# Optimization experiments

Measured on AMD Instinct MI355X. Metric: run time of the kernel, lower is better.

Reference implementation:

```python
import jax, jax.numpy as jnp
import numpy as np

N = 100000      # nodes
E = 1280000     # edges
D_IN = 64       # in_channels
D_OUT = 64      # out_channels
D_EDGE = 16     # edge_dim
NEG_SLOPE = 0.01  # torch F.leaky_relu default


def setup_inputs() -> dict:
    key = jax.random.key(0)
    ks = jax.random.split(key, 8)
    x = jax.random.normal(ks[0], (N, D_IN), dtype=jnp.float32)
    edge_attr = jax.random.normal(ks[1], (E, D_EDGE), dtype=jnp.float32)
    src = jax.random.randint(ks[2], (E,), 0, N, dtype=jnp.int32)
    dst = jax.random.randint(ks[3], (E,), 0, N, dtype=jnp.int32)
    # parameters (xavier-like scale)
    W1 = jax.random.normal(ks[4], (D_OUT, D_IN + D_EDGE), dtype=jnp.float32) * (2.0 / (D_OUT + D_IN + D_EDGE)) ** 0.5
    W2 = jax.random.normal(ks[5], (D_OUT, D_IN), dtype=jnp.float32) * (2.0 / (D_OUT + D_IN)) ** 0.5
    attn = jax.random.normal(ks[6], (D_OUT + D_IN,), dtype=jnp.float32) * (2.0 / (1 + D_OUT + D_IN)) ** 0.5
    bias = jnp.zeros((D_OUT,), dtype=jnp.float32)
    return {"x": x, "edge_attr": edge_attr, "src": src, "dst": dst,
            "W1": W1, "W2": W2, "attn": attn, "bias": bias}


def reference(x, edge_attr, src, dst, W1, W2, attn, bias):
    # node transform: lin2
    x_t = x @ W2.T                                    # [N, D_OUT]
    # per-edge gathers
    x_l = x[src]                                      # [E, D_IN]
    x_r = x[dst]                                      # [E, D_IN]
    # lin1 on [x_l || edge_attr]
    f_srt = jnp.concatenate([x_l, edge_attr], axis=-1) @ W1.T   # [E, D_OUT]
    e = jax.nn.leaky_relu(jnp.concatenate([f_srt, x_r], axis=-1), NEG_SLOPE)  # [E, D_OUT+D_IN]
    logits = e @ attn                                 # [E]
    # edge_softmax over destination-node segments
    seg_max = jax.ops.segment_max(logits, dst, num_segments=N)
    seg_max = jnp.where(jnp.isfinite(seg_max), seg_max, 0.0)
    expd = jnp.exp(logits - seg_max[dst])             # [E]
    denom = jax.ops.segment_sum(expd, dst, num_segments=N)
    alpha = expd / denom[dst]                         # [E]  (dropout p=0 -> identity)
    # scatter-sum aggregation: sum_e alpha_e * x_t[src_e] into dst
    msgs = x_t[src] * alpha[:, None]                  # [E, D_OUT]
    h = jax.ops.segment_sum(msgs, dst, num_segments=N)
    return h + bias
```

## Files before the change

kernel.cpp:

```cpp
#include <hip/hip_runtime.h>

#define D 64
#define D_EDGE 16
#define NEG 0.01f

typedef unsigned int  uint32;
typedef unsigned short ushort16;

__device__ __forceinline__ float leaky(float v) { return fmaxf(v, NEG * v); }

__device__ __forceinline__ ushort16 f2bf(float f) {
    uint32 b = __float_as_uint(f);
    uint32 r = b + 0x7fffu + ((b >> 16) & 1u);
    return (ushort16)(r >> 16);
}
__device__ __forceinline__ float bf2f(ushort16 u) {
    return __uint_as_float(((uint32)u) << 16);
}
__device__ __forceinline__ float bf_lo(uint32 w) { return __uint_as_float(w << 16); }
__device__ __forceinline__ float bf_hi(uint32 w) { return __uint_as_float(w & 0xffff0000u); }

__global__ __launch_bounds__(256) void node_kernel(
    const float* __restrict__ x, const float* __restrict__ W1,
    const float* __restrict__ W2,
    ushort16* __restrict__ Abf, ushort16* __restrict__ xtb, int N_)
{
    __shared__ float xs[64][68];
    uint32* sA = (uint32*)&xs[0][0];
    uint32* sX = sA + 64 * 33;

    const int tid = threadIdx.x;
    const int b0  = blockIdx.x * 64;

    for (int idx = tid; idx < 64 * 16; idx += 256) {
        const int rr = idx >> 4, cc = idx & 15;
        float4 v = make_float4(0.f, 0.f, 0.f, 0.f);
        if (b0 + rr < N_) v = ((const float4*)(x + (size_t)(b0 + rr) * D))[cc];
        *(float4*)&xs[rr][cc * 4] = v;
    }
    __syncthreads();

    const int lane = tid & 63;
    const int q    = __builtin_amdgcn_readfirstlane(tid >> 6);

    float4 xr[16];
#pragma unroll
    for (int i = 0; i < 16; i++) xr[i] = *(const float4*)&xs[lane][4 * i];
    __syncthreads();

    float a_prev = 0.f, b_prev = 0.f;
#pragma unroll
    for (int kk = 0; kk < 16; kk++) {
        const int k = q * 16 + kk;
        const float4* w2r = (const float4*)(W2 + (size_t)k * 64);
        const float4* w1r = (const float4*)(W1 + (size_t)k * 80);
        float a = 0.f, b = 0.f;
#pragma unroll
        for (int j = 0; j < 16; j++) {
            float4 w = w2r[j];
            a += xr[j].x * w.x + xr[j].y * w.y + xr[j].z * w.z + xr[j].w * w.w;
            float4 u = w1r[j];
            b += xr[j].x * u.x + xr[j].y * u.y + xr[j].z * u.z + xr[j].w * u.w;
        }
        if (kk & 1) {
            const int pr = k >> 1;
            sX[lane * 33 + pr] = (uint32)f2bf(a_prev) | ((uint32)f2bf(a) << 16);
            sA[lane * 33 + pr] = (uint32)f2bf(b_prev) | ((uint32)f2bf(b) << 16);
        } else {
            a_prev = a; b_prev = b;
        }
    }
    __syncthreads();

    uint32* Au = (uint32*)Abf;
    uint32* Xu = (uint32*)xtb;
    const size_t gbase = (size_t)b0 * 32;
    for (int base = tid * 4; base < 2048; base += 1024) {
        const int nn = base >> 5, cc = base & 31;
        if (b0 + nn < N_) {
            const uint32* ra = sA + nn * 33 + cc;
            const uint32* rx = sX + nn * 33 + cc;
            uint4 va = make_uint4(ra[0], ra[1], ra[2], ra[3]);
            uint4 vx = make_uint4(rx[0], rx[1], rx[2], rx[3]);
            *(uint4*)(Au + gbase + base) = va;
            *(uint4*)(Xu + gbase + base) = vx;
        }
    }
}

__global__ __launch_bounds__(256) void hist_kernel(
    const int* __restrict__ dst, int* __restrict__ cnt, int E_)
{
    int i = blockIdx.x * 256 + threadIdx.x;
    if (i < E_) atomicAdd(cnt + dst[i], 1);
}

__global__ __launch_bounds__(256) void scan1(
    const int* __restrict__ cnt, int* __restrict__ part, int N_)
{
    __shared__ int sm[256];
    const int b = blockIdx.x, t = threadIdx.x;
    const int i0 = b * 1024 + t * 4;
    int s = 0;
    if (i0     < N_) s += cnt[i0];
    if (i0 + 1 < N_) s += cnt[i0 + 1];
    if (i0 + 2 < N_) s += cnt[i0 + 2];
    if (i0 + 3 < N_) s += cnt[i0 + 3];
    sm[t] = s; __syncthreads();
    for (int off = 128; off > 0; off >>= 1) {
        if (t < off) sm[t] += sm[t + off];
        __syncthreads();
    }
    if (t == 0) part[b] = sm[0];
}

__global__ __launch_bounds__(256) void scan2(int* __restrict__ part, int nb)
{
    __shared__ int sm[256];
    const int t = threadIdx.x;
    int v = (t < nb) ? part[t] : 0;
    sm[t] = v; __syncthreads();
    for (int off = 1; off < 256; off <<= 1) {
        int a = (t >= off) ? sm[t - off] : 0;
        __syncthreads();
        sm[t] += a;
        __syncthreads();
    }
    if (t < nb) part[t] = sm[t] - v;
}

__global__ __launch_bounds__(256) void scan3(
    const int* __restrict__ cnt, const int* __restrict__ part,
    int* __restrict__ rowst, int N_)
{
    __shared__ int sm[256];
    const int b = blockIdx.x, t = threadIdx.x;
    const int i0 = b * 1024 + t * 4;
    int c0 = 0, c1 = 0, c2 = 0, c3 = 0;
    if (i0     < N_) c0 = cnt[i0];
    if (i0 + 1 < N_) c1 = cnt[i0 + 1];
    if (i0 + 2 < N_) c2 = cnt[i0 + 2];
    if (i0 + 3 < N_) c3 = cnt[i0 + 3];
    const int s = c0 + c1 + c2 + c3;
    sm[t] = s; __syncthreads();
    for (int off = 1; off < 256; off <<= 1) {
        int a = (t >= off) ? sm[t - off] : 0;
        __syncthreads();
        sm[t] += a;
        __syncthreads();
    }
    const int base = part[b] + (sm[t] - s);
    if (i0     < N_) rowst[i0]     = base;
    if (i0 + 1 < N_) rowst[i0 + 1] = base + c0;
    if (i0 + 2 < N_) rowst[i0 + 2] = base + c0 + c1;
    if (i0 + 3 < N_) rowst[i0 + 3] = base + c0 + c1 + c2;
}

__global__ __launch_bounds__(256) void edge_kernel(
    const float* __restrict__ edge_attr, const int* __restrict__ src,
    const int* __restrict__ dst, const float* __restrict__ W1,
    const float* __restrict__ attn, const ushort16* __restrict__ Abf,
    int* __restrict__ rowpos, int2* __restrict__ SP, int E_)
{
    const int e = blockIdx.x * 256 + threadIdx.x;
    if (e >= E_) return;

    const int s = src[e];
    const int d = dst[e];

    uint32 Ad[32];
    {
        const uint4* Ap = (const uint4*)(Abf + (size_t)s * D);
#pragma unroll
        for (int i = 0; i < 8; i++) *(uint4*)(Ad + 4 * i) = Ap[i];
    }
    float Ef[16];
    {
        const float4* Ep = (const float4*)(edge_attr + (size_t)e * D_EDGE);
#pragma unroll
        for (int i = 0; i < 4; i++) *(float4*)(Ef + 4 * i) = Ep[i];
    }

    float v = 0.f;
#pragma unroll
    for (int j = 0; j < 32; ++j) {
        const float4* w0 = (const float4*)(W1 + (2 * j) * 80 + 64);
        const float4* w1 = (const float4*)(W1 + (2 * j + 1) * 80 + 64);
        float4 p0 = w0[0], p1 = w0[1], p2 = w0[2], p3 = w0[3];
        float4 q0 = w1[0], q1 = w1[1], q2 = w1[2], q3 = w1[3];

        float g0 = bf_lo(Ad[j]);
        float g1 = bf_hi(Ad[j]);

        g0 = fmaf(Ef[ 0], p0.x, g0); g1 = fmaf(Ef[ 0], q0.x, g1);
        g0 = fmaf(Ef[ 1], p0.y, g0); g1 = fmaf(Ef[ 1], q0.y, g1);
        g0 = fmaf(Ef[ 2], p0.z, g0); g1 = fmaf(Ef[ 2], q0.z, g1);
        g0 = fmaf(Ef[ 3], p0.w, g0); g1 = fmaf(Ef[ 3], q0.w, g1);
        g0 = fmaf(Ef[ 4], p1.x, g0); g1 = fmaf(Ef[ 4], q1.x, g1);
        g0 = fmaf(Ef[ 5], p1.y, g0); g1 = fmaf(Ef[ 5], q1.y, g1);
        g0 = fmaf(Ef[ 6], p1.z, g0); g1 = fmaf(Ef[ 6], q1.z, g1);
        g0 = fmaf(Ef[ 7], p1.w, g0); g1 = fmaf(Ef[ 7], q1.w, g1);
        g0 = fmaf(Ef[ 8], p2.x, g0); g1 = fmaf(Ef[ 8], q2.x, g1);
        g0 = fmaf(Ef[ 9], p2.y, g0); g1 = fmaf(Ef[ 9], q2.y, g1);
        g0 = fmaf(Ef[10], p2.z, g0); g1 = fmaf(Ef[10], q2.z, g1);
        g0 = fmaf(Ef[11], p2.w, g0); g1 = fmaf(Ef[11], q2.w, g1);
        g0 = fmaf(Ef[12], p3.x, g0); g1 = fmaf(Ef[12], q3.x, g1);
        g0 = fmaf(Ef[13], p3.y, g0); g1 = fmaf(Ef[13], q3.y, g1);
        g0 = fmaf(Ef[14], p3.z, g0); g1 = fmaf(Ef[14], q3.z, g1);
        g0 = fmaf(Ef[15], p3.w, g0); g1 = fmaf(Ef[15], q3.w, g1);

        v = fmaf(leaky(g0), attn[2 * j],     v);
        v = fmaf(leaky(g1), attn[2 * j + 1], v);
    }

    const float p = __expf(v);
    const int pos = atomicAdd(rowpos + d, 1);
    SP[pos] = make_int2(s, __float_as_int(p));
}

__global__ __launch_bounds__(256) void agg_kernel(
    const ushort16* __restrict__ xtb, const int2* __restrict__ SP,
    const int* __restrict__ rowend, const float* __restrict__ bias,
    float* __restrict__ out, int N_)
{
    const int n    = blockIdx.x * 4 + (threadIdx.x >> 6);
    const int lane = threadIdx.x & 63;
    if (n >= N_) return;
    const int half = lane >> 5;
    const int c    = lane & 31;

    const int end   = rowend[n];
    const int start = n ? rowend[n - 1] : 0;
    const uint32* X = (const uint32*)xtb;

    float accx = 0.f, accy = 0.f, den = 0.f;
    int i = start;
    for (; i + 7 < end; i += 8) {
        int2 A0 = SP[i+0], A1 = SP[i+1], A2 = SP[i+2], A3 = SP[i+3];
        int2 A4 = SP[i+4], A5 = SP[i+5], A6 = SP[i+6], A7 = SP[i+7];
        int   r0 = half ? A1.x : A0.x;  float p0 = __int_as_float(half ? A1.y : A0.y);
        int   r1 = half ? A3.x : A2.x;  float p1 = __int_as_float(half ? A3.y : A2.y);
        int   r2 = half ? A5.x : A4.x;  float p2 = __int_as_float(half ? A5.y : A4.y);
        int   r3 = half ? A7.x : A6.x;  float p3 = __int_as_float(half ? A7.y : A6.y);
        uint32 u0 = X[(size_t)r0 * 32 + c];
        uint32 u1 = X[(size_t)r1 * 32 + c];
        uint32 u2 = X[(size_t)r2 * 32 + c];
        uint32 u3 = X[(size_t)r3 * 32 + c];
        accx = fmaf(p0, bf_lo(u0), accx); accy = fmaf(p0, bf_hi(u0), accy);
        accx = fmaf(p1, bf_lo(u1), accx); accy = fmaf(p1, bf_hi(u1), accy);
        accx = fmaf(p2, bf_lo(u2), accx); accy = fmaf(p2, bf_hi(u2), accy);
        accx = fmaf(p3, bf_lo(u3), accx); accy = fmaf(p3, bf_hi(u3), accy);
        den += (p0 + p1) + (p2 + p3);
    }
    for (; i < end; i++) {
        int2 a = SP[i];
        if (half == 0) {
            float p = __int_as_float(a.y);
            uint32 u = X[(size_t)a.x * 32 + c];
            accx = fmaf(p, bf_lo(u), accx);
            accy = fmaf(p, bf_hi(u), accy);
            den += p;
        }
    }
    accx += __shfl_xor(accx, 32, 64);
    accy += __shfl_xor(accy, 32, 64);
    den  += __shfl_xor(den,  32, 64);

    if (half == 0) {
        const float sc = den > 0.f ? 1.f / den : 0.f;
        const float2 bb = *(const float2*)(bias + 2 * c);
        float2 o;
        o.x = fmaf(accx, sc, bb.x);
        o.y = fmaf(accy, sc, bb.y);
        *(float2*)(out + (size_t)n * D + 2 * c) = o;
    }
}

extern "C" void kernel_launch(void* const* d_in, const int* in_sizes, int n_in,
                              void* d_out, int out_size, void* d_ws, size_t ws_size,
                              hipStream_t stream)
{
    const float* x         = (const float*)d_in[0];
    const float* edge_attr = (const float*)d_in[1];
    const int*   src       = (const int*)d_in[2];
    const int*   dst       = (const int*)d_in[3];
    const float* W1        = (const float*)d_in[4];
    const float* W2        = (const float*)d_in[5];
    const float* attn      = (const float*)d_in[6];
    const float* bias      = (const float*)d_in[7];
    float* out = (float*)d_out;

    const int N_ = in_sizes[0] / D;
    const int E_ = in_sizes[2];

    char* w = (char*)d_ws;
    ushort16* Abf  = (ushort16*)w;  w += (size_t)N_ * D * sizeof(ushort16);
    ushort16* xtb  = (ushort16*)w;  w += (size_t)N_ * D * sizeof(ushort16);
    int2*     SP   = (int2*)w;      w += (size_t)E_ * sizeof(int2);
    int*      rowst= (int*)w;       w += (size_t)N_ * sizeof(int);
    int*      cnt  = (int*)w;       w += (size_t)N_ * sizeof(int);
    int*      part = (int*)w;

    hipMemsetAsync(cnt, 0, (size_t)N_ * sizeof(int), stream);

    const int NB1 = (N_ + 1023) / 1024;

    hist_kernel<<<(E_ + 255) / 256, 256, 0, stream>>>(dst, cnt, E_);
    scan1<<<NB1, 256, 0, stream>>>(cnt, part, N_);
    scan2<<<1, 256, 0, stream>>>(part, NB1);
    scan3<<<NB1, 256, 0, stream>>>(cnt, part, rowst, N_);

    node_kernel<<<(N_ + 63) / 64, 256, 0, stream>>>(x, W1, W2, Abf, xtb, N_);

    edge_kernel<<<(E_ + 255) / 256, 256, 0, stream>>>(edge_attr, src, dst, W1,
                                                      attn, Abf, rowst, SP, E_);

    agg_kernel<<<(N_ + 3) / 4, 256, 0, stream>>>(xtb, SP, rowst, bias, out, N_);
}
```

Measured before the change: 414.2 us.

## Fold block-prefix scan into scan3 and split edge FMA chains

Removes the separate single-block scan2 launch by having every scan3 block redundantly scan the partial sums in shared memory, which saves one kernel launch and its dependency gap. The edge kernel's per-channel dot products are split into two independent FMA chains with two attention accumulators, to shorten the dependent-FMA latency. It also adds a min-blocks launch bound of 4 to cap register use. The trade-offs are slightly different floating-point summation order and possible register spills under the tighter bound.

Result: no change. 412.2 us (-0.5%).

```diff
diff --git a/kernel.cpp b/kernel.cpp
--- a/kernel.cpp
+++ b/kernel.cpp
@@ -114,27 +114,24 @@
     if (t == 0) part[b] = sm[0];
 }
 
-__global__ __launch_bounds__(256) void scan2(int* __restrict__ part, int nb)
-{
-    __shared__ int sm[256];
-    const int t = threadIdx.x;
-    int v = (t < nb) ? part[t] : 0;
-    sm[t] = v; __syncthreads();
-    for (int off = 1; off < 256; off <<= 1) {
-        int a = (t >= off) ? sm[t - off] : 0;
-        __syncthreads();
-        sm[t] += a;
-        __syncthreads();
-    }
-    if (t < nb) part[t] = sm[t] - v;
-}
-
 __global__ __launch_bounds__(256) void scan3(
     const int* __restrict__ cnt, const int* __restrict__ part,
-    int* __restrict__ rowst, int N_)
-{
+    int* __restrict__ rowst, int N_, int nb)
+{
+    __shared__ int sp[256];
     __shared__ int sm[256];
     const int b = blockIdx.x, t = threadIdx.x;
+
+    sp[t] = (t < nb) ? part[t] : 0;
+    __syncthreads();
+    for (int off = 1; off < 256; off <<= 1) {
+        int a = (t >= off) ? sp[t - off] : 0;
+        __syncthreads();
+        sp[t] += a;
+        __syncthreads();
+    }
+    const int pbase = (b > 0) ? sp[b - 1] : 0;
+
     const int i0 = b * 1024 + t * 4;
     int c0 = 0, c1 = 0, c2 = 0, c3 = 0;
     if (i0     < N_) c0 = cnt[i0];
@@ -149,14 +146,14 @@
         sm[t] += a;
         __syncthreads();
     }
-    const int base = part[b] + (sm[t] - s);
+    const int base = pbase + (sm[t] - s);
     if (i0     < N_) rowst[i0]     = base;
     if (i0 + 1 < N_) rowst[i0 + 1] = base + c0;
     if (i0 + 2 < N_) rowst[i0 + 2] = base + c0 + c1;
     if (i0 + 3 < N_) rowst[i0 + 3] = base + c0 + c1 + c2;
 }
 
-__global__ __launch_bounds__(256) void edge_kernel(
+__global__ __launch_bounds__(256, 4) void edge_kernel(
     const float* __restrict__ edge_attr, const int* __restrict__ src,
     const int* __restrict__ dst, const float* __restrict__ W1,
     const float* __restrict__ attn, const ushort16* __restrict__ Abf,
@@ -181,7 +178,7 @@
         for (int i = 0; i < 4; i++) *(float4*)(Ef + 4 * i) = Ep[i];
     }
 
-    float v = 0.f;
+    float va = 0.f, vb = 0.f;
 #pragma unroll
     for (int j = 0; j < 32; ++j) {
         const float4* w0 = (const float4*)(W1 + (2 * j) * 80 + 64);
@@ -189,31 +186,35 @@
         float4 p0 = w0[0], p1 = w0[1], p2 = w0[2], p3 = w0[3];
         float4 q0 = w1[0], q1 = w1[1], q2 = w1[2], q3 = w1[3];
 
-        float g0 = bf_lo(Ad[j]);
-        float g1 = bf_hi(Ad[j]);
-
-        g0 = fmaf(Ef[ 0], p0.x, g0); g1 = fmaf(Ef[ 0], q0.x, g1);
-        g0 = fmaf(Ef[ 1], p0.y, g0); g1 = fmaf(Ef[ 1], q0.y, g1);
-        g0 = fmaf(Ef[ 2], p0.z, g0); g1 = fmaf(Ef[ 2], q0.z, g1);
-        g0 = fmaf(Ef[ 3], p0.w, g0); g1 = fmaf(Ef[ 3], q0.w, g1);
-        g0 = fmaf(Ef[ 4], p1.x, g0); g1 = fmaf(Ef[ 4], q1.x, g1);
-        g0 = fmaf(Ef[ 5], p1.y, g0); g1 = fmaf(Ef[ 5], q1.y, g1);
-        g0 = fmaf(Ef[ 6], p1.z, g0); g1 = fmaf(Ef[ 6], q1.z, g1);
-        g0 = fmaf(Ef[ 7], p1.w, g0); g1 = fmaf(Ef[ 7], q1.w, g1);
-        g0 = fmaf(Ef[ 8], p2.x, g0); g1 = fmaf(Ef[ 8], q2.x, g1);
-        g0 = fmaf(Ef[ 9], p2.y, g0); g1 = fmaf(Ef[ 9], q2.y, g1);
-        g0 = fmaf(Ef[10], p2.z, g0); g1 = fmaf(Ef[10], q2.z, g1);
-        g0 = fmaf(Ef[11], p2.w, g0); g1 = fmaf(Ef[11], q2.w, g1);
-        g0 = fmaf(Ef[12], p3.x, g0); g1 = fmaf(Ef[12], q3.x, g1);
-        g0 = fmaf(Ef[13], p3.y, g0); g1 = fmaf(Ef[13], q3.y, g1);
-        g0 = fmaf(Ef[14], p3.z, g0); g1 = fmaf(Ef[14], q3.z, g1);
-        g0 = fmaf(Ef[15], p3.w, g0); g1 = fmaf(Ef[15], q3.w, g1);
-
-        v = fmaf(leaky(g0), attn[2 * j],     v);
-        v = fmaf(leaky(g1), attn[2 * j + 1], v);
-    }
-
-    const float p = __expf(v);
+        float c0 = bf_lo(Ad[j]);
+        float c1 = 0.f;
+        c0 = fmaf(Ef[ 0], p0.x, c0); c1 = fmaf(Ef[ 8], p2.x, c1);
+        c0 = fmaf(Ef[ 1], p0.y, c0); c1 = fmaf(Ef[ 9], p2.y, c1);
+        c0 = fmaf(Ef[ 2], p0.z, c0); c1 = fmaf(Ef[10], p2.z, c1);
+        c0 = fmaf(Ef[ 3], p0.w, c0); c1 = fmaf(Ef[11], p2.w, c1);
+        c0 = fmaf(Ef[ 4], p1.x, c0); c1 = fmaf(Ef[12], p3.x, c1);
+        c0 = fmaf(Ef[ 5], p1.y, c0); c1 = fmaf(Ef[13], p3.y, c1);
+        c0 = fmaf(Ef[ 6], p1.z, c0); c1 = fmaf(Ef[14], p3.z, c1);
+        c0 = fmaf(Ef[ 7], p1.w, c0); c1 = fmaf(Ef[15], p3.w, c1);
+        float g0 = c0 + c1;
+
+        float e0 = bf_hi(Ad[j]);
+        float e1 = 0.f;
+        e0 = fmaf(Ef[ 0], q0.x, e0); e1 = fmaf(Ef[ 8], q2.x, e1);
+        e0 = fmaf(Ef[ 1], q0.y, e0); e1 = fmaf(Ef[ 9], q2.y, e1);
+        e0 = fmaf(Ef[ 2], q0.z, e0); e1 = fmaf(Ef[10], q2.z, e1);
+        e0 = fmaf(Ef[ 3], q0.w, e0); e1 = fmaf(Ef[11], q2.w, e1);
+        e0 = fmaf(Ef[ 4], q1.x, e0); e1 = fmaf(Ef[12], q3.x, e1);
+        e0 = fmaf(Ef[ 5], q1.y, e0); e1 = fmaf(Ef[13], q3.y, e1);
+        e0 = fmaf(Ef[ 6], q1.z, e0); e1 = fmaf(Ef[14], q3.z, e1);
+        e0 = fmaf(Ef[ 7], q1.w, e0); e1 = fmaf(Ef[15], q3.w, e1);
+        float g1 = e0 + e1;
+
+        va = fmaf(leaky(g0), attn[2 * j],     va);
+        vb = fmaf(leaky(g1), attn[2 * j + 1], vb);
+    }
+
+    const float p = __expf(va + vb);
     const int pos = atomicAdd(rowpos + d, 1);
     SP[pos] = make_int2(s, __float_as_int(p));
 }
@@ -307,8 +308,7 @@
 
     hist_kernel<<<(E_ + 255) / 256, 256, 0, stream>>>(dst, cnt, E_);
     scan1<<<NB1, 256, 0, stream>>>(cnt, part, N_);
-    scan2<<<1, 256, 0, stream>>>(part, NB1);
-    scan3<<<NB1, 256, 0, stream>>>(cnt, part, rowst, N_);
+    scan3<<<NB1, 256, 0, stream>>>(cnt, part, rowst, N_, NB1);
 
     node_kernel<<<(N_ + 63) / 64, 256, 0, stream>>>(x, W1, W2, Abf, xtb, N_);
 
```
